# Kernel tuning notes

Hardware: AMD Instinct MI355X
Metric: run time of the kernel (lower is better)

## Reference

```python
import jax, jax.numpy as jnp
import numpy as np

B = 16384      # batch
F = 26         # onehot fields
E = 32         # embedding_dim
L = 50         # multihot bag length
V = 1000000    # num_embeddings
CT = 13        # continuous features
D0, D1, D2, D3 = 909, 512, 256, 1
LEAKY = 0.01


def _leaky(x):
    return jnp.where(x >= 0, x, LEAKY * x)


def setup_inputs() -> dict:
    key = jax.random.key(0)
    ks = jax.random.split(key, 16)
    inp = {
        "onehot_i": jax.random.randint(ks[0], (B, F), 0, V),
        "onehot_x": jax.random.uniform(ks[1], (B, F), dtype=jnp.float32),
        "multihot_i1": jax.random.randint(ks[2], (B, L), 0, V),
        "multihot_x1": jax.random.uniform(ks[3], (B, L), dtype=jnp.float32),
        "multihot_i2": jax.random.randint(ks[4], (B, L), 0, V),
        "multihot_x2": jax.random.uniform(ks[5], (B, L), dtype=jnp.float32),
        "ctns": jax.random.normal(ks[6], (B, CT), dtype=jnp.float32),
        # learned parameters
        "wide_table": jax.random.normal(ks[7], (V, 1), dtype=jnp.float32) * 0.02,
        "deep_table": jax.random.normal(ks[8], (V, E), dtype=jnp.float32) * 0.02,
        "w2": jax.random.normal(ks[9], (D1, D0), dtype=jnp.float32) * (1.0 / np.sqrt(D0)),
        "b2": jnp.zeros((D1,), dtype=jnp.float32),
        "w3": jax.random.normal(ks[10], (D2, D1), dtype=jnp.float32) * (1.0 / np.sqrt(D1)),
        "b3": jnp.zeros((D2,), dtype=jnp.float32),
        "w4": jax.random.normal(ks[11], (D3, D2), dtype=jnp.float32) * (1.0 / np.sqrt(D2)),
        "b4": jnp.zeros((D3,), dtype=jnp.float32),
    }
    return inp


def reference(onehot_i, onehot_x, multihot_i1, multihot_x1, multihot_i2,
              multihot_x2, ctns, wide_table, deep_table, w2, b2, w3, b3, w4, b4):
    # ---- wide part ----
    # Original broadcasts the [B,F,1] wide embedding against x repeated E times,
    # then sums over all columns. That equals E * sum_f(w[idx]*x).
    wide_sum = (wide_table[onehot_i, 0] * onehot_x).sum(axis=1)          # [B]
    wide_sum = wide_sum + (wide_table[multihot_i1, 0] * multihot_x1).sum(axis=1)
    wide_sum = wide_sum + (wide_table[multihot_i2, 0] * multihot_x2).sum(axis=1)
    wide_out = E * wide_sum                                              # [B]

    # ---- deep part: gather, scale by field weight, pool multihot bags ----
    d_one = (deep_table[onehot_i] * onehot_x[:, :, None]).reshape(B, F * E)   # [B, F*E]
    d_m1 = (deep_table[multihot_i1] * multihot_x1[:, :, None]).sum(axis=1)    # [B, E]
    d_m2 = (deep_table[multihot_i2] * multihot_x2[:, :, None]).sum(axis=1)    # [B, E]
    x = jnp.concatenate([d_one, d_m1, d_m2, ctns], axis=1)                    # [B, D0]

    # dropout p=0.0 (deterministic reference)
    x = _leaky(x @ w2.T + b2)
    x = _leaky(x @ w3.T + b3)
    x = (x @ w4.T + b4).squeeze(-1)                                           # [B]
    return jax.nn.sigmoid(x + wide_out)
```

## Files before the change

### kernel.cpp

```cpp
#include <hip/hip_runtime.h>
#include <hip/hip_bf16.h>
#include <math.h>

#define B_    16384
#define F_    26
#define E_    32
#define L_    50
#define CT_   13
#define D0_   909
#define KP    960
#define D1_   512
#define D2_   256

#define NEMB  4096
#define W2N   (D1_ * KP)
#define W3N   (D2_ * D1_)
#define CVTB  ((W2N + W3N + 255) / 256)

typedef __bf16 bf16x8 __attribute__((ext_vector_type(8)));
typedef float f32x4 __attribute__((ext_vector_type(4)));

__device__ inline unsigned short f2b(float f) {
    union { __hip_bfloat16 h; unsigned short u; } v;
    v.h = __float2bfloat16(f);
    return v.u;
}
__device__ inline void gld_lds16(const void* g, void* l) {
    __builtin_amdgcn_global_load_lds(
        (const __attribute__((address_space(1))) unsigned int*)g,
        (__attribute__((address_space(3))) unsigned int*)l, 16, 0, 0);
}

__global__ __launch_bounds__(256) void embed_cvt_kernel(
    const int* __restrict__ oi, const float* __restrict__ ox,
    const int* __restrict__ i1, const float* __restrict__ x1,
    const int* __restrict__ i2, const float* __restrict__ x2,
    const float* __restrict__ ct, const float* __restrict__ wtab,
    const float* __restrict__ dtab,
    const float* __restrict__ w2, const float* __restrict__ w3,
    __hip_bfloat16* __restrict__ x0b, float* __restrict__ wid,
    __hip_bfloat16* __restrict__ w2b, __hip_bfloat16* __restrict__ w3b)
{
    const int tid  = threadIdx.x;
    const int lane = tid & 63;
    const int w    = tid >> 6;

    if (blockIdx.x >= NEMB) {
        int i = (blockIdx.x - NEMB) * 256 + tid;
        if (i < W2N) {
            int r = i / KP, c = i - r * KP;
            float v = (c < D0_) ? w2[r * D0_ + c] : 0.f;
            w2b[i] = __float2bfloat16(v);
        } else {
            int j = i - W2N;
            if (j < W3N) w3b[j] = __float2bfloat16(w3[j]);
        }
        return;
    }

    const int s = blockIdx.x * 4 + w;
    const int g = lane >> 3;
    const int l = lane & 7;
    unsigned short* xrow = (unsigned short*)(x0b + (size_t)s * KP);
    const f32x4* dt4 = (const f32x4*)dtab;

    int koh[4]; float soh[4];
#pragma unroll
    for (int t = 0; t < 4; t++) {
        int f = g + 8 * t; bool v = (f < F_);
        koh[t] = v ? oi[s * F_ + f] : 0;
        soh[t] = v ? ox[s * F_ + f] : 0.f;
    }
    int k1[7], k2[7]; float sc1[7], sc2[7];
#pragma unroll
    for (int t = 0; t < 7; t++) {
        int j = g + 8 * t; bool v = (j < L_);
        k1[t]  = v ? i1[s * L_ + j] : 0;
        sc1[t] = v ? x1[s * L_ + j] : 0.f;
        k2[t]  = v ? i2[s * L_ + j] : 0;
        sc2[t] = v ? x2[s * L_ + j] : 0.f;
    }
    f32x4 r1[7], r2[7], roh[4];
#pragma unroll
    for (int t = 0; t < 7; t++) r1[t] = dt4[(size_t)k1[t] * 8 + l];
#pragma unroll
    for (int t = 0; t < 7; t++) r2[t] = dt4[(size_t)k2[t] * 8 + l];
#pragma unroll
    for (int t = 0; t < 4; t++) roh[t] = dt4[(size_t)koh[t] * 8 + l];

#pragma unroll
    for (int t = 0; t < 4; t++) {
        int f = g + 8 * t;
        if (f < F_) {
            ushort4 o;
            o.x = f2b(roh[t].x * soh[t]); o.y = f2b(roh[t].y * soh[t]);
            o.z = f2b(roh[t].z * soh[t]); o.w = f2b(roh[t].w * soh[t]);
            *(ushort4*)(xrow + f * E_ + l * 4) = o;
        }
    }
    f32x4 a1 = {0.f,0.f,0.f,0.f}, a2 = {0.f,0.f,0.f,0.f};
#pragma unroll
    for (int t = 0; t < 7; t++) {
        a1.x = fmaf(r1[t].x, sc1[t], a1.x); a1.y = fmaf(r1[t].y, sc1[t], a1.y);
        a1.z = fmaf(r1[t].z, sc1[t], a1.z); a1.w = fmaf(r1[t].w, sc1[t], a1.w);
        a2.x = fmaf(r2[t].x, sc2[t], a2.x); a2.y = fmaf(r2[t].y, sc2[t], a2.y);
        a2.z = fmaf(r2[t].z, sc2[t], a2.z); a2.w = fmaf(r2[t].w, sc2[t], a2.w);
    }
#pragma unroll
    for (int m = 8; m < 64; m <<= 1) {
        a1.x += __shfl_xor(a1.x, m); a1.y += __shfl_xor(a1.y, m);
        a1.z += __shfl_xor(a1.z, m); a1.w += __shfl_xor(a1.w, m);
        a2.x += __shfl_xor(a2.x, m); a2.y += __shfl_xor(a2.y, m);
        a2.z += __shfl_xor(a2.z, m); a2.w += __shfl_xor(a2.w, m);
    }
    if (g == 0) {
        ushort4 o; o.x = f2b(a1.x); o.y = f2b(a1.y); o.z = f2b(a1.z); o.w = f2b(a1.w);
        *(ushort4*)(xrow + F_ * E_ + l * 4) = o;
    }
    if (g == 1) {
        ushort4 o; o.x = f2b(a2.x); o.y = f2b(a2.y); o.z = f2b(a2.z); o.w = f2b(a2.w);
        *(ushort4*)(xrow + F_ * E_ + E_ + l * 4) = o;
    }
    {
        float v = (lane < CT_) ? ct[s * CT_ + lane] : 0.f;
        xrow[F_ * E_ + 2 * E_ + lane] = f2b(v);
    }
    float acc = 0.f;
#pragma unroll
    for (int t = lane; t < F_ + 2 * L_; t += 64) {
        int idx; float xv;
        if (t < F_)            { idx = oi[s * F_ + t];           xv = ox[s * F_ + t]; }
        else if (t < F_ + L_)  { int j = t - F_;      idx = i1[s * L_ + j]; xv = x1[s * L_ + j]; }
        else                   { int j = t - F_ - L_; idx = i2[s * L_ + j]; xv = x2[s * L_ + j]; }
        acc += wtab[idx] * xv;
    }
    for (int o = 32; o; o >>= 1) acc += __shfl_xor(acc, o);
    if (lane == 0) wid[s] = (float)E_ * acc;
}

__global__ __launch_bounds__(256) void gemm1_kernel(
    const __hip_bfloat16* __restrict__ A,
    const __hip_bfloat16* __restrict__ W,
    const float* __restrict__ bias,
    __hip_bfloat16* __restrict__ C)
{
    __shared__ __hip_bfloat16 As[2][128 * 32];
    __shared__ __hip_bfloat16 Bs[2][128 * 32];

    const int bm   = blockIdx.x & 127;
    const int bn   = blockIdx.x >> 7;
    const int tid  = threadIdx.x;
    const int lane = tid & 63;
    const int w    = tid >> 6;
    const int wm   = w >> 1, wn = w & 1;

    f32x4 acc[4][4] = {};

    const int srow = lane >> 2;
    const int scol = (lane & 3) * 8;
    const __hip_bfloat16* Aw0 = A + ((size_t)bm * 128 + w * 32 + srow) * KP + scol;
    const __hip_bfloat16* Aw1 = Aw0 + (size_t)16 * KP;
    const __hip_bfloat16* Ww0 = W + ((size_t)bn * 128 + w * 32 + srow) * KP + scol;
    const __hip_bfloat16* Ww1 = Ww0 + (size_t)16 * KP;
    char* AsW = (char*)As + w * 2048;
    char* BsW = (char*)Bs + w * 2048;

    const int fr = lane & 15;
    const int kg = (lane >> 4) * 8;

    for (int k0 = 0; k0 < KP; k0 += 64) {
#pragma unroll
        for (int p = 0; p < 2; p++) {
            gld_lds16(Aw0 + k0 + p * 32, AsW + p * 8192);
            gld_lds16(Aw1 + k0 + p * 32, AsW + p * 8192 + 1024);
            gld_lds16(Ww0 + k0 + p * 32, BsW + p * 8192);
            gld_lds16(Ww1 + k0 + p * 32, BsW + p * 8192 + 1024);
        }
        __syncthreads();

#pragma unroll
        for (int p = 0; p < 2; p++) {
            bf16x8 af[4], bfv[4];
#pragma unroll
            for (int i = 0; i < 4; i++)
                af[i] = *(const bf16x8*)(As[p] + (wm * 64 + i * 16 + fr) * 32 + kg);
#pragma unroll
            for (int i = 0; i < 4; i++)
                bfv[i] = *(const bf16x8*)(Bs[p] + (wn * 64 + i * 16 + fr) * 32 + kg);
#pragma unroll
            for (int i = 0; i < 4; i++)
#pragma unroll
                for (int j = 0; j < 4; j++)
                    acc[i][j] = __builtin_amdgcn_mfma_f32_16x16x32_bf16(af[i], bfv[j], acc[i][j], 0, 0, 0);
        }
        __syncthreads();
    }

    float bv[4];
#pragma unroll
    for (int j = 0; j < 4; j++) bv[j] = bias[bn * 128 + wn * 64 + j * 16 + fr];
    const int crow0 = bm * 128 + wm * 64 + (lane >> 4) * 4;
    const int ccol0 = bn * 128 + wn * 64 + fr;
#pragma unroll
    for (int i = 0; i < 4; i++)
#pragma unroll
        for (int j = 0; j < 4; j++)
#pragma unroll
            for (int r = 0; r < 4; r++) {
                float v = acc[i][j][r] + bv[j];
                v = (v >= 0.f) ? v : 0.01f * v;
                C[(size_t)(crow0 + i * 16 + r) * D1_ + ccol0 + j * 16] = __float2bfloat16(v);
            }
}

__global__ __launch_bounds__(256) void g2f_kernel(
    const __hip_bfloat16* __restrict__ h1b, const __hip_bfloat16* __restrict__ w3b,
    const float* __restrict__ b3, const float* __restrict__ w4,
    const float* __restrict__ b4, const float* __restrict__ wid,
    float* __restrict__ out)
{
    __shared__ __align__(16) __hip_bfloat16 As2[2][64 * 32];
    __shared__ __align__(16) __hip_bfloat16 Bs2[2][256 * 32];
    __shared__ float parts[256];

    const int tid  = threadIdx.x;
    const int lane = tid & 63;
    const int w    = tid >> 6;
    const int r0   = blockIdx.x * 64;

    f32x4 acc[4][4] = {};
    const int srow = lane >> 2;
    const int scol = (lane & 3) * 8;
    const int fr = lane & 15;
    const int kg = (lane >> 4) * 8;

    for (int k0 = 0; k0 < D1_; k0 += 64) {
#pragma unroll
        for (int p = 0; p < 2; p++) {
            gld_lds16(h1b + ((size_t)r0 + w * 16 + srow) * D1_ + k0 + p * 32 + scol,
                      (char*)As2 + p * 4096 + w * 1024);
#pragma unroll
            for (int rr = 0; rr < 4; rr++)
                gld_lds16(w3b + ((size_t)w * 64 + rr * 16 + srow) * D1_ + k0 + p * 32 + scol,
                          (char*)Bs2 + p * 16384 + w * 4096 + rr * 1024);
        }
        __syncthreads();
#pragma unroll
        for (int p = 0; p < 2; p++) {
            bf16x8 af[4], bfv[4];
#pragma unroll
            for (int i = 0; i < 4; i++)
                af[i] = *(const bf16x8*)(As2[p] + (i * 16 + fr) * 32 + kg);
#pragma unroll
            for (int j = 0; j < 4; j++)
                bfv[j] = *(const bf16x8*)(Bs2[p] + (w * 64 + j * 16 + fr) * 32 + kg);
#pragma unroll
            for (int i = 0; i < 4; i++)
#pragma unroll
                for (int j = 0; j < 4; j++)
                    acc[i][j] = __builtin_amdgcn_mfma_f32_16x16x32_bf16(af[i], bfv[j], acc[i][j], 0, 0, 0);
        }
        __syncthreads();
    }

    float p4[4][4];
#pragma unroll
    for (int i = 0; i < 4; i++)
#pragma unroll
        for (int r = 0; r < 4; r++) p4[i][r] = 0.f;
#pragma unroll
    for (int j = 0; j < 4; j++) {
        int n = w * 64 + j * 16 + fr;
        float bb = b3[n];
        float wv = w4[n];
#pragma unroll
        for (int i = 0; i < 4; i++)
#pragma unroll
            for (int r = 0; r < 4; r++) {
                float v = acc[i][j][r] + bb;
                v = (v >= 0.f) ? v : 0.01f * v;
                p4[i][r] = fmaf(v, wv, p4[i][r]);
            }
    }
#pragma unroll
    for (int m = 1; m < 16; m <<= 1)
#pragma unroll
        for (int i = 0; i < 4; i++)
#pragma unroll
            for (int r = 0; r < 4; r++) p4[i][r] += __shfl_xor(p4[i][r], m);
    if (fr == 0) {
        int kq = lane >> 4;
#pragma unroll
        for (int i = 0; i < 4; i++)
#pragma unroll
            for (int r = 0; r < 4; r++)
                parts[w * 64 + i * 16 + kq * 4 + r] = p4[i][r];
    }
    __syncthreads();
    if (tid < 64) {
        float x = parts[tid] + parts[64 + tid] + parts[128 + tid] + parts[192 + tid]
                + b4[0] + wid[r0 + tid];
        out[r0 + tid] = 1.f / (1.f + expf(-x));
    }
}

extern "C" void kernel_launch(void* const* d_in, const int* in_sizes, int n_in,
                              void* d_out, int out_size, void* d_ws, size_t ws_size,
                              hipStream_t stream) {
    const int*   oi  = (const int*)  d_in[0];
    const float* ox  = (const float*)d_in[1];
    const int*   i1  = (const int*)  d_in[2];
    const float* x1  = (const float*)d_in[3];
    const int*   i2  = (const int*)  d_in[4];
    const float* x2  = (const float*)d_in[5];
    const float* ct  = (const float*)d_in[6];
    const float* wt  = (const float*)d_in[7];
    const float* dt  = (const float*)d_in[8];
    const float* w2  = (const float*)d_in[9];
    const float* b2  = (const float*)d_in[10];
    const float* w3  = (const float*)d_in[11];
    const float* b3  = (const float*)d_in[12];
    const float* w4  = (const float*)d_in[13];
    const float* b4  = (const float*)d_in[14];
    float* out = (float*)d_out;

    char* ws = (char*)d_ws;
    __hip_bfloat16* x0b = (__hip_bfloat16*)(ws);
    __hip_bfloat16* h1b = (__hip_bfloat16*)(ws + 31457280);
    float*          wid = (float*)         (ws + 48234496);
    __hip_bfloat16* w2b = (__hip_bfloat16*)(ws + 48300032);
    __hip_bfloat16* w3b = (__hip_bfloat16*)(ws + 49283072);

    embed_cvt_kernel<<<NEMB + CVTB, 256, 0, stream>>>(
        oi, ox, i1, x1, i2, x2, ct, wt, dt, w2, w3, x0b, wid, w2b, w3b);
    gemm1_kernel<<<512, 256, 0, stream>>>(x0b, w2b, b2, h1b);
    g2f_kernel<<<256, 256, 0, stream>>>(h1b, w3b, b3, w4, b4, wid, out);
}
```

Measured before the change: 114.7 us.

## Fuse GEMM1 and GEMM2 into one persistent launch with per-row-tile atomic flags

Merges the first-layer GEMM and the second-layer GEMM plus head into one kernel. Blocks 0-511 compute h1 tiles and release-increment a per-128-row counter. Blocks 512-767 spin until the four column tiles of their row block are done, then run layer two and the sigmoid output. This removes a kernel launch boundary and lets layer two start on finished row blocks while other GEMM1 tiles are still running. In exchange it adds a memset, atomic signalling and spin-waits, and it depends on the GEMM1 blocks being scheduled before the waiting blocks to avoid deadlock.

```diff
diff --git a/kernel.cpp b/kernel.cpp
--- a/kernel.cpp
+++ b/kernel.cpp
@@ -16,6 +16,8 @@
 #define W2N   (D1_ * KP)
 #define W3N   (D2_ * D1_)
 #define CVTB  ((W2N + W3N + 255) / 256)
+#define NG1   512
+#define NG2   256
 
 typedef __bf16 bf16x8 __attribute__((ext_vector_type(8)));
 typedef float f32x4 __attribute__((ext_vector_type(4)));
@@ -138,169 +140,175 @@
     if (lane == 0) wid[s] = (float)E_ * acc;
 }
 
-__global__ __launch_bounds__(256) void gemm1_kernel(
-    const __hip_bfloat16* __restrict__ A,
-    const __hip_bfloat16* __restrict__ W,
-    const float* __restrict__ bias,
-    __hip_bfloat16* __restrict__ C)
+__global__ __launch_bounds__(256) void mlp_sync_kernel(
+    const __hip_bfloat16* __restrict__ x0b,
+    const __hip_bfloat16* __restrict__ w2b, const float* __restrict__ b2,
+    __hip_bfloat16* __restrict__ h1b,
+    const __hip_bfloat16* __restrict__ w3b, const float* __restrict__ b3,
+    const float* __restrict__ w4, const float* __restrict__ b4,
+    const float* __restrict__ wid, int* __restrict__ h1cnt,
+    float* __restrict__ out)
 {
-    __shared__ __hip_bfloat16 As[2][128 * 32];
-    __shared__ __hip_bfloat16 Bs[2][128 * 32];
-
-    const int bm   = blockIdx.x & 127;
-    const int bn   = blockIdx.x >> 7;
+    __shared__ __align__(16) char smem[43008];
     const int tid  = threadIdx.x;
     const int lane = tid & 63;
     const int w    = tid >> 6;
-    const int wm   = w >> 1, wn = w & 1;
-
-    f32x4 acc[4][4] = {};
-
+    const int fr   = lane & 15;
+    const int kg   = (lane >> 4) * 8;
     const int srow = lane >> 2;
     const int scol = (lane & 3) * 8;
-    const __hip_bfloat16* Aw0 = A + ((size_t)bm * 128 + w * 32 + srow) * KP + scol;
-    const __hip_bfloat16* Aw1 = Aw0 + (size_t)16 * KP;
-    const __hip_bfloat16* Ww0 = W + ((size_t)bn * 128 + w * 32 + srow) * KP + scol;
-    const __hip_bfloat16* Ww1 = Ww0 + (size_t)16 * KP;
-    char* AsW = (char*)As + w * 2048;
-    char* BsW = (char*)Bs + w * 2048;
-
-    const int fr = lane & 15;
-    const int kg = (lane >> 4) * 8;
-
-    for (int k0 = 0; k0 < KP; k0 += 64) {
-#pragma unroll
-        for (int p = 0; p < 2; p++) {
-            gld_lds16(Aw0 + k0 + p * 32, AsW + p * 8192);
-            gld_lds16(Aw1 + k0 + p * 32, AsW + p * 8192 + 1024);
-            gld_lds16(Ww0 + k0 + p * 32, BsW + p * 8192);
-            gld_lds16(Ww1 + k0 + p * 32, BsW + p * 8192 + 1024);
-        }
+
+    if (blockIdx.x < NG1) {
+        const int bm = blockIdx.x & 127;
+        const int bn = blockIdx.x >> 7;
+        const int wm = w >> 1, wn = w & 1;
+        f32x4 acc[4][4] = {};
+
+        const __hip_bfloat16* Aw0 = x0b + ((size_t)bm * 128 + w * 32 + srow) * KP + scol;
+        const __hip_bfloat16* Aw1 = Aw0 + (size_t)16 * KP;
+        const __hip_bfloat16* Ww0 = w2b + ((size_t)bn * 128 + w * 32 + srow) * KP + scol;
+        const __hip_bfloat16* Ww1 = Ww0 + (size_t)16 * KP;
+        char* AsW = smem + w * 2048;
+        char* BsW = smem + 16384 + w * 2048;
+
+        for (int k0 = 0; k0 < KP; k0 += 64) {
+#pragma unroll
+            for (int p = 0; p < 2; p++) {
+                gld_lds16(Aw0 + k0 + p * 32, AsW + p * 8192);
+                gld_lds16(Aw1 + k0 + p * 32, AsW + p * 8192 + 1024);
+                gld_lds16(Ww0 + k0 + p * 32, BsW + p * 8192);
+                gld_lds16(Ww1 + k0 + p * 32, BsW + p * 8192 + 1024);
+            }
+            __syncthreads();
+#pragma unroll
+            for (int p = 0; p < 2; p++) {
+                const __hip_bfloat16* Ap = (const __hip_bfloat16*)(smem + p * 8192);
+                const __hip_bfloat16* Bp = (const __hip_bfloat16*)(smem + 16384 + p * 8192);
+                bf16x8 af[4], bfv[4];
+#pragma unroll
+                for (int i = 0; i < 4; i++)
+                    af[i] = *(const bf16x8*)(Ap + (wm * 64 + i * 16 + fr) * 32 + kg);
+#pragma unroll
+                for (int i = 0; i < 4; i++)
+                    bfv[i] = *(const bf16x8*)(Bp + (wn * 64 + i * 16 + fr) * 32 + kg);
+#pragma unroll
+                for (int i = 0; i < 4; i++)
+#pragma unroll
+                    for (int j = 0; j < 4; j++)
+                        acc[i][j] = __builtin_amdgcn_mfma_f32_16x16x32_bf16(af[i], bfv[j], acc[i][j], 0, 0, 0);
+            }
+            __syncthreads();
+        }
+
+        float bv[4];
+#pragma unroll
+        for (int j = 0; j < 4; j++) bv[j] = b2[bn * 128 + wn * 64 + j * 16 + fr];
+        const int crow0 = bm * 128 + wm * 64 + (lane >> 4) * 4;
+        const int ccol0 = bn * 128 + wn * 64 + fr;
+#pragma unroll
+        for (int i = 0; i < 4; i++)
+#pragma unroll
+            for (int j = 0; j < 4; j++)
+#pragma unroll
+                for (int r = 0; r < 4; r++) {
+                    float v = acc[i][j][r] + bv[j];
+                    v = (v >= 0.f) ? v : 0.01f * v;
+                    h1b[(size_t)(crow0 + i * 16 + r) * D1_ + ccol0 + j * 16] = __float2bfloat16(v);
+                }
         __syncthreads();
-
-#pragma unroll
-        for (int p = 0; p < 2; p++) {
-            bf16x8 af[4], bfv[4];
+        if (tid == 0) {
+            __threadfence();
+            __hip_atomic_fetch_add(h1cnt + bm * 16, 1,
+                                   __ATOMIC_RELEASE, __HIP_MEMORY_SCOPE_AGENT);
+        }
+        return;
+    }
+
+    {
+        const int gid2 = blockIdx.x - NG1;
+        const int r0   = gid2 * 64;
+        const int bm   = gid2 >> 1;
+        if (tid == 0) {
+            while (__hip_atomic_load(h1cnt + bm * 16, __ATOMIC_ACQUIRE,
+                                     __HIP_MEMORY_SCOPE_AGENT) < 4)
+                __builtin_amdgcn_s_sleep(16);
+        }
+        __syncthreads();
+        __threadfence();
+
+        float* parts = (float*)(smem + 40960);
+        f32x4 acc[4][4] = {};
+
+        for (int k0 = 0; k0 < D1_; k0 += 64) {
+#pragma unroll
+            for (int p = 0; p < 2; p++) {
+                gld_lds16(h1b + ((size_t)r0 + w * 16 + srow) * D1_ + k0 + p * 32 + scol,
+                          smem + p * 4096 + w * 1024);
+#pragma unroll
+                for (int rr = 0; rr < 4; rr++)
+                    gld_lds16(w3b + ((size_t)w * 64 + rr * 16 + srow) * D1_ + k0 + p * 32 + scol,
+                              smem + 8192 + p * 16384 + w * 4096 + rr * 1024);
+            }
+            __syncthreads();
+#pragma unroll
+            for (int p = 0; p < 2; p++) {
+                const __hip_bfloat16* Ap = (const __hip_bfloat16*)(smem + p * 4096);
+                const __hip_bfloat16* Bp = (const __hip_bfloat16*)(smem + 8192 + p * 16384);
+                bf16x8 af[4], bfv[4];
+#pragma unroll
+                for (int i = 0; i < 4; i++)
+                    af[i] = *(const bf16x8*)(Ap + (i * 16 + fr) * 32 + kg);
+#pragma unroll
+                for (int j = 0; j < 4; j++)
+                    bfv[j] = *(const bf16x8*)(Bp + (w * 64 + j * 16 + fr) * 32 + kg);
+#pragma unroll
+                for (int i = 0; i < 4; i++)
+#pragma unroll
+                    for (int j = 0; j < 4; j++)
+                        acc[i][j] = __builtin_amdgcn_mfma_f32_16x16x32_bf16(af[i], bfv[j], acc[i][j], 0, 0, 0);
+            }
+            __syncthreads();
+        }
+
+        float p4[4][4];
+#pragma unroll
+        for (int i = 0; i < 4; i++)
+#pragma unroll
+            for (int r = 0; r < 4; r++) p4[i][r] = 0.f;
+#pragma unroll
+        for (int j = 0; j < 4; j++) {
+            int n = w * 64 + j * 16 + fr;
+            float bb = b3[n];
+            float wv = w4[n];
 #pragma unroll
             for (int i = 0; i < 4; i++)
-                af[i] = *(const bf16x8*)(As[p] + (wm * 64 + i * 16 + fr) * 32 + kg);
+#pragma unroll
+                for (int r = 0; r < 4; r++) {
+                    float v = acc[i][j][r] + bb;
+                    v = (v >= 0.f) ? v : 0.01f * v;
+                    p4[i][r] = fmaf(v, wv, p4[i][r]);
+                }
+        }
+#pragma unroll
+        for (int m = 1; m < 16; m <<= 1)
 #pragma unroll
             for (int i = 0; i < 4; i++)
-                bfv[i] = *(const bf16x8*)(Bs[p] + (wn * 64 + i * 16 + fr) * 32 + kg);
+#pragma unroll
+                for (int r = 0; r < 4; r++) p4[i][r] += __shfl_xor(p4[i][r], m);
+        if (fr == 0) {
+            int kq = lane >> 4;
 #pragma unroll
             for (int i = 0; i < 4; i++)
 #pragma unroll
-                for (int j = 0; j < 4; j++)
-                    acc[i][j] = __builtin_amdgcn_mfma_f32_16x16x32_bf16(af[i], bfv[j], acc[i][j], 0, 0, 0);
+                for (int r = 0; r < 4; r++)
+                    parts[w * 64 + i * 16 + kq * 4 + r] = p4[i][r];
         }
         __syncthreads();
-    }
-
-    float bv[4];
-#pragma unroll
-    for (int j = 0; j < 4; j++) bv[j] = bias[bn * 128 + wn * 64 + j * 16 + fr];
-    const int crow0 = bm * 128 + wm * 64 + (lane >> 4) * 4;
-    const int ccol0 = bn * 128 + wn * 64 + fr;
-#pragma unroll
-    for (int i = 0; i < 4; i++)
-#pragma unroll
-        for (int j = 0; j < 4; j++)
-#pragma unroll
-            for (int r = 0; r < 4; r++) {
-                float v = acc[i][j][r] + bv[j];
-                v = (v >= 0.f) ? v : 0.01f * v;
-                C[(size_t)(crow0 + i * 16 + r) * D1_ + ccol0 + j * 16] = __float2bfloat16(v);
-            }
-}
-
-__global__ __launch_bounds__(256) void g2f_kernel(
-    const __hip_bfloat16* __restrict__ h1b, const __hip_bfloat16* __restrict__ w3b,
-    const float* __restrict__ b3, const float* __restrict__ w4,
-    const float* __restrict__ b4, const float* __restrict__ wid,
-    float* __restrict__ out)
-{
-    __shared__ __align__(16) __hip_bfloat16 As2[2][64 * 32];
-    __shared__ __align__(16) __hip_bfloat16 Bs2[2][256 * 32];
-    __shared__ float parts[256];
-
-    const int tid  = threadIdx.x;
-    const int lane = tid & 63;
-    const int w    = tid >> 6;
-    const int r0   = blockIdx.x * 64;
-
-    f32x4 acc[4][4] = {};
-    const int srow = lane >> 2;
-    const int scol = (lane & 3) * 8;
-    const int fr = lane & 15;
-    const int kg = (lane >> 4) * 8;
-
-    for (int k0 = 0; k0 < D1_; k0 += 64) {
-#pragma unroll
-        for (int p = 0; p < 2; p++) {
-            gld_lds16(h1b + ((size_t)r0 + w * 16 + srow) * D1_ + k0 + p * 32 + scol,
-                      (char*)As2 + p * 4096 + w * 1024);
-#pragma unroll
-            for (int rr = 0; rr < 4; rr++)
-                gld_lds16(w3b + ((size_t)w * 64 + rr * 16 + srow) * D1_ + k0 + p * 32 + scol,
-                          (char*)Bs2 + p * 16384 + w * 4096 + rr * 1024);
-        }
-        __syncthreads();
-#pragma unroll
-        for (int p = 0; p < 2; p++) {
-            bf16x8 af[4], bfv[4];
-#pragma unroll
-            for (int i = 0; i < 4; i++)
-                af[i] = *(const bf16x8*)(As2[p] + (i * 16 + fr) * 32 + kg);
-#pragma unroll
-            for (int j = 0; j < 4; j++)
-                bfv[j] = *(const bf16x8*)(Bs2[p] + (w * 64 + j * 16 + fr) * 32 + kg);
-#pragma unroll
-            for (int i = 0; i < 4; i++)
-#pragma unroll
-                for (int j = 0; j < 4; j++)
-                    acc[i][j] = __builtin_amdgcn_mfma_f32_16x16x32_bf16(af[i], bfv[j], acc[i][j], 0, 0, 0);
-        }
-        __syncthreads();
-    }
-
-    float p4[4][4];
-#pragma unroll
-    for (int i = 0; i < 4; i++)
-#pragma unroll
-        for (int r = 0; r < 4; r++) p4[i][r] = 0.f;
-#pragma unroll
-    for (int j = 0; j < 4; j++) {
-        int n = w * 64 + j * 16 + fr;
-        float bb = b3[n];
-        float wv = w4[n];
-#pragma unroll
-        for (int i = 0; i < 4; i++)
-#pragma unroll
-            for (int r = 0; r < 4; r++) {
-                float v = acc[i][j][r] + bb;
-                v = (v >= 0.f) ? v : 0.01f * v;
-                p4[i][r] = fmaf(v, wv, p4[i][r]);
-            }
-    }
-#pragma unroll
-    for (int m = 1; m < 16; m <<= 1)
-#pragma unroll
-        for (int i = 0; i < 4; i++)
-#pragma unroll
-            for (int r = 0; r < 4; r++) p4[i][r] += __shfl_xor(p4[i][r], m);
-    if (fr == 0) {
-        int kq = lane >> 4;
-#pragma unroll
-        for (int i = 0; i < 4; i++)
-#pragma unroll
-            for (int r = 0; r < 4; r++)
-                parts[w * 64 + i * 16 + kq * 4 + r] = p4[i][r];
-    }
-    __syncthreads();
-    if (tid < 64) {
-        float x = parts[tid] + parts[64 + tid] + parts[128 + tid] + parts[192 + tid]
-                + b4[0] + wid[r0 + tid];
-        out[r0 + tid] = 1.f / (1.f + expf(-x));
+        if (tid < 64) {
+            float x = parts[tid] + parts[64 + tid] + parts[128 + tid] + parts[192 + tid]
+                    + b4[0] + wid[r0 + tid];
+            out[r0 + tid] = 1.f / (1.f + expf(-x));
+        }
     }
 }
 
@@ -325,14 +333,16 @@
     float* out = (float*)d_out;
 
     char* ws = (char*)d_ws;
-    __hip_bfloat16* x0b = (__hip_bfloat16*)(ws);
-    __hip_bfloat16* h1b = (__hip_bfloat16*)(ws + 31457280);
-    float*          wid = (float*)         (ws + 48234496);
-    __hip_bfloat16* w2b = (__hip_bfloat16*)(ws + 48300032);
-    __hip_bfloat16* w3b = (__hip_bfloat16*)(ws + 49283072);
-
+    __hip_bfloat16* x0b  = (__hip_bfloat16*)(ws);
+    __hip_bfloat16* h1b  = (__hip_bfloat16*)(ws + 31457280);
+    float*          wid  = (float*)         (ws + 48234496);
+    __hip_bfloat16* w2b  = (__hip_bfloat16*)(ws + 48300032);
+    __hip_bfloat16* w3b  = (__hip_bfloat16*)(ws + 49283072);
+    int*            h1c  = (int*)           (ws + 49545216);
+
+    hipMemsetAsync(h1c, 0, 8192, stream);
     embed_cvt_kernel<<<NEMB + CVTB, 256, 0, stream>>>(
         oi, ox, i1, x1, i2, x2, ct, wt, dt, w2, w3, x0b, wid, w2b, w3b);
-    gemm1_kernel<<<512, 256, 0, stream>>>(x0b, w2b, b2, h1b);
-    g2f_kernel<<<256, 256, 0, stream>>>(h1b, w3b, b3, w4, b4, wid, out);
-}
+    mlp_sync_kernel<<<NG1 + NG2, 256, 0, stream>>>(
+        x0b, w2b, b2, h1b, w3b, b3, w4, b4, wid, h1c, out);
+}
```

Result: slower. 178.9 us (+55.9%).
